# Kernel optimization log

Measured on AMD Instinct MI355X. Metric: run time of the kernel, lower is better.

## Reference

```python
import jax, jax.numpy as jnp
import numpy as np

N_NODES = 50000
IN_CH = 128
HIDDEN = 256
N_EDGES = 800000


def setup_inputs() -> dict:
    key = jax.random.key(0)
    k_z, k_e, k_w1, k_b1, k_w2, k_b2 = jax.random.split(key, 6)
    z = jax.random.normal(k_z, (N_NODES, IN_CH), dtype=jnp.float32)
    edge_index = jax.random.randint(k_e, (2, N_EDGES), 0, N_NODES, dtype=jnp.int64)
    # nn.Linear params (stored as [in, out] for x @ W + b)
    lim1 = 1.0 / np.sqrt(2 * IN_CH)
    W1 = jax.random.uniform(k_w1, (2 * IN_CH, HIDDEN), minval=-lim1, maxval=lim1, dtype=jnp.float32)
    b1 = jax.random.uniform(k_b1, (HIDDEN,), minval=-lim1, maxval=lim1, dtype=jnp.float32)
    lim2 = 1.0 / np.sqrt(HIDDEN)
    W2 = jax.random.uniform(k_w2, (HIDDEN, 1), minval=-lim2, maxval=lim2, dtype=jnp.float32)
    b2 = jax.random.uniform(k_b2, (1,), minval=-lim2, maxval=lim2, dtype=jnp.float32)
    return {"z": z, "edge_index": edge_index, "W1": W1, "b1": b1, "W2": W2, "b2": b2}


def reference(z, edge_index, W1, b1, W2, b2):
    row, col = edge_index[0], edge_index[1]
    # gather endpoint embeddings and concat -> [E, 2*in_ch]
    edge_features = jnp.concatenate([z[row], z[col]], axis=1)
    h = jax.nn.relu(edge_features @ W1 + b1)   # [E, hidden]
    logits = (h @ W2 + b2).squeeze(-1)         # [E]
    return jax.nn.sigmoid(logits)
```

## Files before the change

kernel.cpp:

```cpp
#include <hip/hip_runtime.h>
#include <hip/hip_bf16.h>
#include <cstdint>
#include <cstddef>

#define N_EDGES_C 800000
#define N_NODES_C 50000
#define IN_CH_C   128
#define KDIM      256
#define HIDDEN_C  256
#define TM        32
#define NBLK      512
#define THREADS   512

typedef __attribute__((ext_vector_type(8))) short sh8;
typedef __attribute__((ext_vector_type(4))) float f32x4;

__device__ __forceinline__ unsigned short f2bf(float f) {
  union { float f; unsigned u; } a; a.f = f;
  unsigned r = a.u + 0x7fffu + ((a.u >> 16) & 1u);
  return (unsigned short)(r >> 16);
}

__device__ __forceinline__ void glds16(const unsigned short* g, void* l) {
  __builtin_amdgcn_global_load_lds(
      (const __attribute__((address_space(1))) unsigned int*)g,
      (__attribute__((address_space(3))) unsigned int*)l, 16, 0, 0);
}

__global__ void cvt_z_kernel(const float* __restrict__ z,
                             unsigned short* __restrict__ zb) {
  int i = blockIdx.x * blockDim.x + threadIdx.x;
  float4 v = reinterpret_cast<const float4*>(z)[i];
  ushort4 o;
  o.x = f2bf(v.x); o.y = f2bf(v.y); o.z = f2bf(v.z); o.w = f2bf(v.w);
  reinterpret_cast<ushort4*>(zb)[i] = o;
}

__global__ void cvt_w1t_kernel(const float* __restrict__ w1,
                               unsigned short* __restrict__ w1t) {
  int k = blockIdx.x;
  int n = threadIdx.x;
  w1t[(size_t)n * KDIM + k] = f2bf(w1[(size_t)k * HIDDEN_C + n]);
}

__global__ __launch_bounds__(THREADS, 4) void decoder_persist(
    const unsigned short* __restrict__ zb,
    const int* __restrict__ ei,
    const unsigned short* __restrict__ w1t,
    const float* __restrict__ b1,
    const float* __restrict__ w2,
    const float* __restrict__ b2,
    float* __restrict__ out)
{
  __shared__ __align__(16) unsigned char lds[3 * 16384 + 2048];
  float* red = (float*)(lds + 3 * 16384);

  const int tid = threadIdx.x;
  const int w   = tid >> 6;
  const int l   = tid & 63;
  const int l15 = l & 15;
  const int lg  = l >> 4;
  const int n0  = w * 32;

  const int b    = blockIdx.x;
  const bool big = (b < 424);
  const int ntb  = big ? 49 : 48;
  const int S    = big ? (49 * b) : (49 * 424 + 48 * (b - 424));
  const int tb   = S * TM;

  const int nd   = (l >> 4) & 1;
  const int eo0  = 4 * w + (l >> 5);
  const int eo1  = eo0 + 2;
  const int sc   = (l & 31) * 16;
  const int off0 = (sc ^ ((eo0 & 7) << 4)) & 255;
  const int off1 = (sc ^ ((eo1 & 7) << 4)) & 255;
  const int* eip0 = ei + (size_t)nd * N_EDGES_C + tb + eo0;
  const int* eip1 = ei + (size_t)nd * N_EDGES_C + tb + eo1;

  sh8 bfr[2][8];
#pragma unroll
  for (int nt = 0; nt < 2; ++nt)
#pragma unroll
    for (int kk = 0; kk < 8; ++kk)
      bfr[nt][kk] = *reinterpret_cast<const sh8*>(
          w1t + (size_t)(n0 + nt * 16 + l15) * KDIM + kk * 32 + lg * 8);

  const float b1v0 = b1[n0 + l15],      b1v1 = b1[n0 + 16 + l15];
  const float w2v0 = w2[n0 + l15],      w2v1 = w2[n0 + 16 + l15];
  const float b2v  = b2[0];

  const int b2b = (l15 >> 2) & 1;
  const int Eb  = l15 * 512 + 64 * b2b + ((lg * 16) ^ ((l15 & 3) << 4));
  const int Ob  = Eb - 128 * b2b;

  int ia0 = eip0[0],      ia1 = eip1[0];
  __builtin_amdgcn_sched_barrier(0);
  int ib0 = eip0[TM],     ib1 = eip1[TM];
  __builtin_amdgcn_sched_barrier(0);
  glds16(zb + (size_t)ia0 * IN_CH_C + (off0 >> 1), lds + 0 * 16384 + (2 * w + 0) * 1024);
  glds16(zb + (size_t)ia1 * IN_CH_C + (off1 >> 1), lds + 0 * 16384 + (2 * w + 1) * 1024);
  __builtin_amdgcn_sched_barrier(0);
  int jc0 = eip0[2 * TM], jc1 = eip1[2 * TM];
  __builtin_amdgcn_sched_barrier(0);
  glds16(zb + (size_t)ib0 * IN_CH_C + (off0 >> 1), lds + 1 * 16384 + (2 * w + 0) * 1024);
  glds16(zb + (size_t)ib1 * IN_CH_C + (off1 >> 1), lds + 1 * 16384 + (2 * w + 1) * 1024);
  __builtin_amdgcn_sched_barrier(0);

  int cur = 0, nx1 = 16384, nx2 = 32768;

#pragma unroll 1
  for (int t = 0; t < ntb; ++t) {
    __builtin_amdgcn_sched_barrier(0);
    asm volatile("s_waitcnt vmcnt(4) lgkmcnt(0)" ::: "memory");
    __builtin_amdgcn_s_barrier();
    __builtin_amdgcn_sched_barrier(0);

    const int tn = (t + 3 < ntb) ? (t + 3) : (ntb - 1);
    int ni0 = eip0[tn * TM];
    int ni1 = eip1[tn * TM];
    __builtin_amdgcn_sched_barrier(0);

    glds16(zb + (size_t)jc0 * IN_CH_C + (off0 >> 1), lds + nx2 + (2 * w + 0) * 1024);
    glds16(zb + (size_t)jc1 * IN_CH_C + (off1 >> 1), lds + nx2 + (2 * w + 1) * 1024);
    __builtin_amdgcn_sched_barrier(0);

    const f32x4 fz = {0.f, 0.f, 0.f, 0.f};
    f32x4 acc[2][2] = {{fz, fz}, {fz, fz}};
    __builtin_amdgcn_s_setprio(1);
#pragma unroll
    for (int kk = 0; kk < 8; ++kk) {
      const int kb_ = ((kk & 1) ? Ob : Eb) + kk * 64;
#pragma unroll
      for (int mt = 0; mt < 2; ++mt) {
        const sh8 af = *reinterpret_cast<const sh8*>(lds + cur + kb_ + mt * 8192);
        acc[mt][0] = __builtin_amdgcn_mfma_f32_16x16x32_bf16(af, bfr[0][kk], acc[mt][0], 0, 0, 0);
        acc[mt][1] = __builtin_amdgcn_mfma_f32_16x16x32_bf16(af, bfr[1][kk], acc[mt][1], 0, 0, 0);
      }
    }
    __builtin_amdgcn_s_setprio(0);

    float pl[2][4];
#pragma unroll
    for (int mt = 0; mt < 2; ++mt)
#pragma unroll
      for (int r = 0; r < 4; ++r) {
        float v0 = fmaxf(acc[mt][0][r] + b1v0, 0.f);
        float v1 = fmaxf(acc[mt][1][r] + b1v1, 0.f);
        pl[mt][r] = v0 * w2v0 + v1 * w2v1;
      }
#pragma unroll
    for (int s = 1; s < 16; s <<= 1)
#pragma unroll
      for (int mt = 0; mt < 2; ++mt)
#pragma unroll
        for (int r = 0; r < 4; ++r)
          pl[mt][r] += __shfl_xor(pl[mt][r], s, 64);
    if (l15 == 0) {
#pragma unroll
      for (int mt = 0; mt < 2; ++mt) {
        float4 v = make_float4(pl[mt][0], pl[mt][1], pl[mt][2], pl[mt][3]);
        *reinterpret_cast<float4*>(&red[(t & 1) * 256 + w * 32 + mt * 16 + lg * 4]) = v;
      }
    }

    if (t > 0 && tid < TM) {
      float s = b2v;
#pragma unroll
      for (int ww = 0; ww < 8; ++ww)
        s += red[((t - 1) & 1) * 256 + ww * 32 + tid];
      out[tb + (t - 1) * TM + tid] = 1.f / (1.f + __expf(-s));
    }

    jc0 = ni0; jc1 = ni1;
    int tmp = cur; cur = nx1; nx1 = nx2; nx2 = tmp;
  }

  __builtin_amdgcn_sched_barrier(0);
  asm volatile("s_waitcnt lgkmcnt(0)" ::: "memory");
  __builtin_amdgcn_s_barrier();
  __builtin_amdgcn_sched_barrier(0);
  if (tid < TM) {
    float s = b2v;
#pragma unroll
    for (int ww = 0; ww < 8; ++ww)
      s += red[((ntb - 1) & 1) * 256 + ww * 32 + tid];
    out[tb + (ntb - 1) * TM + tid] = 1.f / (1.f + __expf(-s));
  }
  asm volatile("s_waitcnt vmcnt(0)" ::: "memory");
}

#define BM 64
__global__ __launch_bounds__(512, 6) void decoder_fb(
    const float* __restrict__ z, const int* __restrict__ ei,
    const unsigned short* __restrict__ w1t, const float* __restrict__ b1,
    const float* __restrict__ w2, const float* __restrict__ b2,
    float* __restrict__ out)
{
  __shared__ __align__(16) unsigned char lds[BM * 512];
  const int tid = threadIdx.x, wave = tid >> 6, lane = tid & 63;
  const int l15 = lane & 15, lg = lane >> 4, base = blockIdx.x * BM;
  {
    const int e = tid & 63, w8 = tid >> 6, nd = w8 >> 2;
    const int idx = ei[nd * N_EDGES_C + base + e];
    const int swzw = (e & 7) << 4;
    char* dstrow = (char*)lds + e * 512;
    const float* src = z + (size_t)idx * IN_CH_C + (w8 & 3) * 32;
    float4 tf[8];
#pragma unroll
    for (int i = 0; i < 8; ++i) tf[i] = reinterpret_cast<const float4*>(src)[i];
#pragma unroll
    for (int i = 0; i < 4; ++i) {
      sh8 o; const float4 x0 = tf[2*i], x1 = tf[2*i+1];
      o[0]=(short)f2bf(x0.x); o[1]=(short)f2bf(x0.y); o[2]=(short)f2bf(x0.z); o[3]=(short)f2bf(x0.w);
      o[4]=(short)f2bf(x1.x); o[5]=(short)f2bf(x1.y); o[6]=(short)f2bf(x1.z); o[7]=(short)f2bf(x1.w);
      *reinterpret_cast<sh8*>(dstrow + ((w8 * 64 + i * 16) ^ swzw)) = o;
    }
  }
  __syncthreads();
  const int n0 = wave * 32;
  const int swz = (l15 & 7) << 4;
  const int Ebase = l15 * 512 + ((lg * 16) ^ swz);
  const int Obase = Ebase - ((swz & 64) << 1);
  const f32x4 fz = {0.f,0.f,0.f,0.f};
  f32x4 acc[4][2];
#pragma unroll
  for (int mt = 0; mt < 4; ++mt) { acc[mt][0] = fz; acc[mt][1] = fz; }
#pragma unroll
  for (int kk = 0; kk < 8; ++kk) {
    const int kOff = kk * 32 + lg * 8;
    sh8 bfrag[2];
#pragma unroll
    for (int nt = 0; nt < 2; ++nt)
      bfrag[nt] = *reinterpret_cast<const sh8*>(w1t + (size_t)(n0 + nt*16 + l15) * KDIM + kOff);
    const int kbase = ((kk & 1) ? Obase : Ebase) + kk * 64;
#pragma unroll
    for (int mt = 0; mt < 4; ++mt) {
      const sh8 af = *reinterpret_cast<const sh8*>((char*)lds + (kbase + mt * 8192));
      acc[mt][0] = __builtin_amdgcn_mfma_f32_16x16x32_bf16(af, bfrag[0], acc[mt][0], 0, 0, 0);
      acc[mt][1] = __builtin_amdgcn_mfma_f32_16x16x32_bf16(af, bfrag[1], acc[mt][1], 0, 0, 0);
    }
  }
  float plog[4][4];
#pragma unroll
  for (int mt = 0; mt < 4; ++mt)
#pragma unroll
    for (int r = 0; r < 4; ++r) plog[mt][r] = 0.f;
#pragma unroll
  for (int nt = 0; nt < 2; ++nt) {
    const int j = n0 + nt * 16 + l15;
    const float b1v = b1[j], w2v = w2[j];
#pragma unroll
    for (int mt = 0; mt < 4; ++mt)
#pragma unroll
      for (int r = 0; r < 4; ++r)
        plog[mt][r] = fmaf(fmaxf(acc[mt][nt][r] + b1v, 0.f), w2v, plog[mt][r]);
  }
#pragma unroll
  for (int s = 1; s < 16; s <<= 1)
#pragma unroll
    for (int mt = 0; mt < 4; ++mt)
#pragma unroll
      for (int r = 0; r < 4; ++r)
        plog[mt][r] += __shfl_xor(plog[mt][r], s, 64);
  __syncthreads();
  float* red = (float*)lds;
  if (l15 == 0)
#pragma unroll
    for (int mt = 0; mt < 4; ++mt)
#pragma unroll
      for (int r = 0; r < 4; ++r)
        red[wave * 64 + mt * 16 + lg * 4 + r] = plog[mt][r];
  __syncthreads();
  if (tid < BM) {
    float s = b2[0];
#pragma unroll
    for (int w = 0; w < 8; ++w) s += red[w * 64 + tid];
    out[base + tid] = 1.f / (1.f + __expf(-s));
  }
}

extern "C" void kernel_launch(void* const* d_in, const int* in_sizes, int n_in,
                              void* d_out, int out_size, void* d_ws, size_t ws_size,
                              hipStream_t stream) {
  const float* z  = (const float*)d_in[0];
  const int*   ei = (const int*)d_in[1];
  const float* W1 = (const float*)d_in[2];
  const float* b1 = (const float*)d_in[3];
  const float* W2 = (const float*)d_in[4];
  const float* b2 = (const float*)d_in[5];
  float* out = (float*)d_out;

  unsigned short* w1t = (unsigned short*)d_ws;
  const size_t w1t_bytes = (size_t)HIDDEN_C * KDIM * sizeof(unsigned short);
  unsigned short* zb = (unsigned short*)((char*)d_ws + w1t_bytes);
  const size_t need = w1t_bytes + (size_t)N_NODES_C * IN_CH_C * sizeof(unsigned short);
  const bool zbf = (ws_size >= need);

  cvt_w1t_kernel<<<KDIM, HIDDEN_C, 0, stream>>>(W1, w1t);
  if (zbf) {
    const int n4 = N_NODES_C * IN_CH_C / 4;
    cvt_z_kernel<<<n4 / 256, 256, 0, stream>>>(z, zb);
    decoder_persist<<<NBLK, THREADS, 0, stream>>>(zb, ei, w1t, b1, W2, b2, out);
  } else {
    decoder_fb<<<N_EDGES_C / BM, 512, 0, stream>>>(z, ei, w1t, b1, W2, b2, out);
  }
}
```

Baseline: 158.4 us.

## Precompute per-node W1 projections and reduce edges to gather-add-relu-dot

Splits the first linear layer algebraically: each node's embedding is multiplied once by the top and bottom halves of W1 (with bias folded in) and stored in bf16, so per-edge work becomes gathering two 256-wide vectors, adding, ReLU, and a dot with W2. This replaces the per-edge 256x256 GEMM with a per-node GEMM over 50k nodes, removing most of the matrix work. The cost is a larger workspace (a 50k x 512 bf16 table) and extra rounding, since the pre-activation sums are stored in bf16. The old persistent path is kept as a fallback when the workspace is too small.

Result: slower. 214.2 us (+35.2%).

```diff
diff --git a/kernel.cpp b/kernel.cpp
--- a/kernel.cpp
+++ b/kernel.cpp
@@ -8,9 +8,6 @@
 #define IN_CH_C   128
 #define KDIM      256
 #define HIDDEN_C  256
-#define TM        32
-#define NBLK      512
-#define THREADS   512
 
 typedef __attribute__((ext_vector_type(8))) short sh8;
 typedef __attribute__((ext_vector_type(4))) float f32x4;
@@ -20,6 +17,142 @@
   unsigned r = a.u + 0x7fffu + ((a.u >> 16) & 1u);
   return (unsigned short)(r >> 16);
 }
+
+
+__global__ void cvt_w1ct_kernel(const float* __restrict__ w1,
+                                unsigned short* __restrict__ w1ct) {
+  int k = blockIdx.x;
+  int j = threadIdx.x;
+  float v = (j < 256) ? w1[(size_t)k * 256 + j]
+                      : w1[(size_t)(128 + k) * 256 + (j - 256)];
+  w1ct[(size_t)j * 128 + k] = f2bf(v);
+}
+
+__global__ __launch_bounds__(512) void build_zw_kernel(
+    const float* __restrict__ z,
+    const unsigned short* __restrict__ w1ct,
+    const float* __restrict__ b1,
+    unsigned short* __restrict__ zw)
+{
+  const int tid  = threadIdx.x;
+  const int wave = tid >> 6;
+  const int l    = tid & 63;
+  const int l15  = l & 15;
+  const int lg   = l >> 4;
+  const int nb   = blockIdx.x;
+  const int j0   = wave * 64;
+
+  sh8 bfr[4][4];
+#pragma unroll
+  for (int nt = 0; nt < 4; ++nt)
+#pragma unroll
+    for (int kk = 0; kk < 4; ++kk)
+      bfr[nt][kk] = *reinterpret_cast<const sh8*>(
+          w1ct + (size_t)(j0 + nt * 16 + l15) * 128 + kk * 32 + lg * 8);
+
+  const f32x4 fz = {0.f, 0.f, 0.f, 0.f};
+  f32x4 acc[4][4];
+#pragma unroll
+  for (int mt = 0; mt < 4; ++mt)
+#pragma unroll
+    for (int nt = 0; nt < 4; ++nt)
+      acc[mt][nt] = fz;
+
+#pragma unroll
+  for (int kk = 0; kk < 4; ++kk) {
+#pragma unroll
+    for (int mt = 0; mt < 4; ++mt) {
+      int node = nb * 64 + mt * 16 + l15;
+      node = (node < N_NODES_C) ? node : (N_NODES_C - 1);
+      const float* zp = z + (size_t)node * IN_CH_C + kk * 32 + lg * 8;
+      const float4 x0 = reinterpret_cast<const float4*>(zp)[0];
+      const float4 x1 = reinterpret_cast<const float4*>(zp)[1];
+      sh8 af;
+      af[0] = (short)f2bf(x0.x); af[1] = (short)f2bf(x0.y);
+      af[2] = (short)f2bf(x0.z); af[3] = (short)f2bf(x0.w);
+      af[4] = (short)f2bf(x1.x); af[5] = (short)f2bf(x1.y);
+      af[6] = (short)f2bf(x1.z); af[7] = (short)f2bf(x1.w);
+#pragma unroll
+      for (int nt = 0; nt < 4; ++nt)
+        acc[mt][nt] = __builtin_amdgcn_mfma_f32_16x16x32_bf16(
+            af, bfr[nt][kk], acc[mt][nt], 0, 0, 0);
+    }
+  }
+
+#pragma unroll
+  for (int nt = 0; nt < 4; ++nt) {
+    const int j = j0 + nt * 16 + l15;
+    const float bb = (j < 256) ? b1[j] : 0.f;
+#pragma unroll
+    for (int mt = 0; mt < 4; ++mt) {
+#pragma unroll
+      for (int r = 0; r < 4; ++r) {
+        const int node = nb * 64 + mt * 16 + lg * 4 + r;
+        if (node < N_NODES_C)
+          zw[(size_t)node * 512 + j] = f2bf(acc[mt][nt][r] + bb);
+      }
+    }
+  }
+}
+
+__global__ __launch_bounds__(256) void edge_pass_kernel(
+    const unsigned short* __restrict__ zw,
+    const int* __restrict__ ei,
+    const float* __restrict__ w2,
+    const float* __restrict__ b2,
+    float* __restrict__ out)
+{
+  const int tid = threadIdx.x;
+  const int w   = tid >> 6;
+  const int l   = tid & 63;
+  const int g   = l >> 3;
+  const int q   = l & 7;
+  const int e   = blockIdx.x * 32 + w * 8 + g;
+
+  float w2v[32];
+#pragma unroll
+  for (int i = 0; i < 8; ++i) {
+    const float4 v = reinterpret_cast<const float4*>(w2 + q * 32)[i];
+    w2v[i * 4 + 0] = v.x; w2v[i * 4 + 1] = v.y;
+    w2v[i * 4 + 2] = v.z; w2v[i * 4 + 3] = v.w;
+  }
+
+  const int r = ei[e];
+  const int c = ei[N_EDGES_C + e];
+
+  const uint4* tp = reinterpret_cast<const uint4*>(zw + (size_t)r * 512 + q * 32);
+  const uint4* bp = reinterpret_cast<const uint4*>(zw + (size_t)c * 512 + 256 + q * 32);
+  uint4 T[4], B[4];
+#pragma unroll
+  for (int i = 0; i < 4; ++i) T[i] = tp[i];
+#pragma unroll
+  for (int i = 0; i < 4; ++i) B[i] = bp[i];
+
+  const unsigned* Tu = reinterpret_cast<const unsigned*>(T);
+  const unsigned* Bu = reinterpret_cast<const unsigned*>(B);
+
+  float a0 = 0.f, a1 = 0.f;
+#pragma unroll
+  for (int i = 0; i < 16; ++i) {
+    const unsigned u = Tu[i], v = Bu[i];
+    float lo = __uint_as_float(u << 16) + __uint_as_float(v << 16);
+    float hi = __uint_as_float(u & 0xffff0000u) + __uint_as_float(v & 0xffff0000u);
+    lo = fmaxf(lo, 0.f);
+    hi = fmaxf(hi, 0.f);
+    a0 = fmaf(lo, w2v[2 * i], a0);
+    a1 = fmaf(hi, w2v[2 * i + 1], a1);
+  }
+  float s = a0 + a1;
+  s += __shfl_xor(s, 1, 64);
+  s += __shfl_xor(s, 2, 64);
+  s += __shfl_xor(s, 4, 64);
+  if (q == 0)
+    out[e] = 1.f / (1.f + __expf(-(s + b2[0])));
+}
+
+#define TM        32
+#define NBLK      512
+#define THREADS   512
 
 __device__ __forceinline__ void glds16(const unsigned short* g, void* l) {
   __builtin_amdgcn_global_load_lds(
@@ -290,18 +423,27 @@
   const float* b2 = (const float*)d_in[5];
   float* out = (float*)d_out;
 
-  unsigned short* w1t = (unsigned short*)d_ws;
-  const size_t w1t_bytes = (size_t)HIDDEN_C * KDIM * sizeof(unsigned short);
-  unsigned short* zb = (unsigned short*)((char*)d_ws + w1t_bytes);
-  const size_t need = w1t_bytes + (size_t)N_NODES_C * IN_CH_C * sizeof(unsigned short);
-  const bool zbf = (ws_size >= need);
-
-  cvt_w1t_kernel<<<KDIM, HIDDEN_C, 0, stream>>>(W1, w1t);
-  if (zbf) {
-    const int n4 = N_NODES_C * IN_CH_C / 4;
-    cvt_z_kernel<<<n4 / 256, 256, 0, stream>>>(z, zb);
+  const size_t w1_bytes  = (size_t)512 * 128 * sizeof(unsigned short);
+  const size_t zw_bytes  = (size_t)N_NODES_C * 512 * sizeof(unsigned short);
+  const size_t zb_bytes  = (size_t)N_NODES_C * IN_CH_C * sizeof(unsigned short);
+  const size_t need_primary = w1_bytes + zw_bytes;
+  const size_t need_middle  = w1_bytes + zb_bytes;
+
+  if (ws_size >= need_primary) {
+    unsigned short* w1ct = (unsigned short*)d_ws;
+    unsigned short* zw   = (unsigned short*)((char*)d_ws + w1_bytes);
+    cvt_w1ct_kernel<<<128, 512, 0, stream>>>(W1, w1ct);
+    build_zw_kernel<<<(N_NODES_C + 63) / 64, 512, 0, stream>>>(z, w1ct, b1, zw);
+    edge_pass_kernel<<<N_EDGES_C / 32, 256, 0, stream>>>(zw, ei, W2, b2, out);
+  } else if (ws_size >= need_middle) {
+    unsigned short* w1t = (unsigned short*)d_ws;
+    unsigned short* zb  = (unsigned short*)((char*)d_ws + w1_bytes);
+    cvt_w1t_kernel<<<KDIM, HIDDEN_C, 0, stream>>>(W1, w1t);
+    cvt_z_kernel<<<(N_NODES_C * IN_CH_C / 4) / 256, 256, 0, stream>>>(z, zb);
     decoder_persist<<<NBLK, THREADS, 0, stream>>>(zb, ei, w1t, b1, W2, b2, out);
   } else {
+    unsigned short* w1t = (unsigned short*)d_ws;
+    cvt_w1t_kernel<<<KDIM, HIDDEN_C, 0, stream>>>(W1, w1t);
     decoder_fb<<<N_EDGES_C / BM, 512, 0, stream>>>(z, ei, w1t, b1, W2, b2, out);
   }
 }
```
